# Kernel optimization log

Measured on AMD Instinct MI355X. Metric: run time of the kernel, lower is better.

Reference implementation:

```python
import jax, jax.numpy as jnp
import numpy as np

HEADS = 4


def _forward(x_atoms, pos, edge_attr, molecular_features, emb_W, emb_b, mp_W1, mp_b1, mp_W2, mp_b2, ln_g, ln_b, attn_in_w, attn_in_b, attn_out_w, attn_out_b, pool_W, pool_b, mol_gate, lrn_gate, molemb_W1, molemb_b1, molemb_W2, molemb_b2, lrnemb_W1, lrnemb_b1, lrnemb_W2, lrnemb_b2, fus_W1, fus_b1, fus_W2, fus_b2, head_W1, head_b1, head_W2, head_b2, edge_index, batch_idx):
    N = x_atoms.shape[0]
    B = molecular_features.shape[0]
    A = N // B  # equal-size molecules; batch_idx = repeat(arange(B), A)
    H = emb_W.shape[1]
    L = mp_W1.shape[0]
    src, dst = edge_index[0], edge_index[1]  # PyG: x_j = x[src], x_i = x[dst]
    x = x_atoms @ emb_W + emb_b
    # distance features (constant across layers)
    diff = pos[dst] - pos[src]
    d = jnp.sqrt(jnp.sum(diff * diff, axis=1, keepdims=True) + 1e-12)
    dist_feat = jnp.concatenate([d, 1.0 / (1.0 + d), jnp.exp(-d)], axis=1)  # [E,3]
    ones_e = jnp.ones((src.shape[0], 1), x.dtype)
    cnt = jnp.maximum(jax.ops.segment_sum(ones_e, dst, num_segments=N), 1.0)
    for l in range(L):
        res = x
        msg = jnp.concatenate([x[dst], x[src], dist_feat], axis=1)  # [E, 2H+3]
        msg = jax.nn.relu(msg @ mp_W1[l] + mp_b1[l]) @ mp_W2[l] + mp_b2[l]
        x = jax.ops.segment_sum(msg, dst, num_segments=N) / cnt  # mean aggregation
        y = x + res
        mu = y.mean(-1, keepdims=True)
        var = jnp.var(y, axis=-1, keepdims=True)
        x = (y - mu) * jax.lax.rsqrt(var + 1e-5) * ln_g[l] + ln_b[l]
    xm = x.reshape(B, A, H)
    explicit = xm.mean(axis=1)  # scatter_mean over equal-size graphs
    # per-molecule multi-head self-attention (torch MHA, eval mode)
    hd = H // HEADS
    qkv = xm @ attn_in_w.T + attn_in_b
    q, k, v = jnp.split(qkv, 3, axis=-1)
    q = q.reshape(B, A, HEADS, hd)
    k = k.reshape(B, A, HEADS, hd)
    v = v.reshape(B, A, HEADS, hd)
    scores = jnp.einsum('bqhd,bkhd->bhqk', q, k) / jnp.sqrt(jnp.asarray(hd, x.dtype))
    att = jax.nn.softmax(scores, axis=-1)
    o = jnp.einsum('bhqk,bkhd->bqhd', att, v).reshape(B, A, H)
    attended = o @ attn_out_w.T + attn_out_b
    aw = jax.nn.softmax(jnp.sum(attended * xm, axis=-1), axis=1)  # [B,A]
    wmean = jnp.sum(attended * aw[..., None], axis=1)
    maxp = attended.max(axis=1)
    meanp = attended.mean(axis=1)
    stdp = jnp.std(attended, axis=1, ddof=1)  # torch.std unbiased
    pooled = jnp.stack([wmean, maxp, meanp, stdp], axis=0)  # [4,B,H]
    proj = jnp.einsum('kbh,khf->kbf', pooled, pool_W) + pool_b[:, None, :]
    learned = jnp.moveaxis(proj, 0, 1).reshape(B, -1)  # [B,LF]
    # per-property gated MLPs, vectorized over P (atom gates are computed but unused in the source)
    gm = molecular_features[None] * jax.nn.sigmoid(mol_gate)[:, None, :]
    gl = learned[None] * jax.nn.sigmoid(lrn_gate)[:, None, :]
    molrep = jax.nn.relu(jnp.einsum('pbm,pmh->pbh', gm, molemb_W1) + molemb_b1[:, None, :])
    molrep = jnp.einsum('pbh,phk->pbk', molrep, molemb_W2) + molemb_b2[:, None, :]
    lrnrep = jax.nn.relu(jnp.einsum('pbm,pmh->pbh', gl, lrnemb_W1) + lrnemb_b1[:, None, :])
    lrnrep = jnp.einsum('pbh,phk->pbk', lrnrep, lrnemb_W2) + lrnemb_b2[:, None, :]
    P = mol_gate.shape[0]
    comb = jnp.concatenate([jnp.broadcast_to(explicit[None], (P, B, H)), molrep, lrnrep], axis=-1)
    fused = jax.nn.relu(jnp.einsum('pbc,pch->pbh', comb, fus_W1) + fus_b1[:, None, :])
    fused = jnp.einsum('pbh,phk->pbk', fused, fus_W2) + fus_b2[:, None, :]
    h = jax.nn.relu(jnp.einsum('pbh,phk->pbk', fused, head_W1) + head_b1[:, None, :])
    out = jnp.einsum('pbk,pko->pbo', h, head_W2) + head_b2[:, None, :]
    return out  # [P,B,1]: stacked predictions for the 4 properties


def setup_inputs() -> dict:
    key = jax.random.key(0)
    ks = jax.random.split(key, 24)
    B, A, F, M, H, LF, L, P = 1024, 32, 64, 200, 128, 64, 3, 4
    N = B * A
    E = N * 16
    H2, H4, Q = H // 2, H // 4, LF // 4
    n = lambda i, shape, s=1.0: jax.random.normal(ks[i], shape, dtype=jnp.float32) * s
    inp = {}
    inp['x_atoms'] = n(0, (N, F))
    inp['pos'] = n(1, (N, 3)) * 3.0
    inp['edge_attr'] = n(2, (E, 4))
    inp['molecular_features'] = n(3, (B, M))
    inp['emb_W'] = n(4, (F, H), 0.1)
    inp['emb_b'] = jnp.zeros((H,), jnp.float32)
    inp['mp_W1'] = n(5, (L, 2 * H + 3, H), 0.05)
    inp['mp_b1'] = jnp.zeros((L, H), jnp.float32)
    inp['mp_W2'] = n(6, (L, H, H), 0.05)
    inp['mp_b2'] = jnp.zeros((L, H), jnp.float32)
    inp['ln_g'] = jnp.ones((L, H), jnp.float32)
    inp['ln_b'] = jnp.zeros((L, H), jnp.float32)
    inp['attn_in_w'] = n(7, (3 * H, H), 0.08)
    inp['attn_in_b'] = jnp.zeros((3 * H,), jnp.float32)
    inp['attn_out_w'] = n(8, (H, H), 0.08)
    inp['attn_out_b'] = jnp.zeros((H,), jnp.float32)
    inp['pool_W'] = n(9, (4, H, Q), 0.08)
    inp['pool_b'] = jnp.zeros((4, Q), jnp.float32)
    inp['mol_gate'] = n(10, (P, M))
    inp['lrn_gate'] = n(11, (P, LF))
    inp['molemb_W1'] = n(12, (P, M, H2), 0.08)
    inp['molemb_b1'] = jnp.zeros((P, H2), jnp.float32)
    inp['molemb_W2'] = n(13, (P, H2, H2), 0.08)
    inp['molemb_b2'] = jnp.zeros((P, H2), jnp.float32)
    inp['lrnemb_W1'] = n(14, (P, LF, H2), 0.08)
    inp['lrnemb_b1'] = jnp.zeros((P, H2), jnp.float32)
    inp['lrnemb_W2'] = n(15, (P, H2, H2), 0.08)
    inp['lrnemb_b2'] = jnp.zeros((P, H2), jnp.float32)
    inp['fus_W1'] = n(16, (P, 2 * H, H), 0.08)
    inp['fus_b1'] = jnp.zeros((P, H), jnp.float32)
    inp['fus_W2'] = n(17, (P, H, H2), 0.08)
    inp['fus_b2'] = jnp.zeros((P, H2), jnp.float32)
    inp['head_W1'] = n(18, (P, H2, H4), 0.08)
    inp['head_b1'] = jnp.zeros((P, H4), jnp.float32)
    inp['head_W2'] = n(19, (P, H4, 1), 0.08)
    inp['head_b2'] = jnp.zeros((P, 1), jnp.float32)
    inp['edge_index'] = jax.random.randint(ks[20], (2, E), 0, N)
    inp['batch_idx'] = jnp.repeat(jnp.arange(B), A)
    return inp


def reference(x_atoms, pos, edge_attr, molecular_features, emb_W, emb_b, mp_W1, mp_b1, mp_W2, mp_b2, ln_g, ln_b, attn_in_w, attn_in_b, attn_out_w, attn_out_b, pool_W, pool_b, mol_gate, lrn_gate, molemb_W1, molemb_b1, molemb_W2, molemb_b2, lrnemb_W1, lrnemb_b1, lrnemb_W2, lrnemb_b2, fus_W1, fus_b1, fus_W2, fus_b2, head_W1, head_b1, head_W2, head_b2, edge_index, batch_idx):
    return _forward(x_atoms, pos, edge_attr, molecular_features, emb_W, emb_b, mp_W1, mp_b1, mp_W2, mp_b2, ln_g, ln_b, attn_in_w, attn_in_b, attn_out_w, attn_out_b, pool_W, pool_b, mol_gate, lrn_gate, molemb_W1, molemb_b1, molemb_W2, molemb_b2, lrnemb_W1, lrnemb_b1, lrnemb_W2, lrnemb_b2, fus_W1, fus_b1, fus_W2, fus_b2, head_W1, head_b1, head_W2, head_b2, edge_index, batch_idx)
```

## Files before the change

kernel.cpp:

```cpp
#include <hip/hip_runtime.h>

#define NE 524288
#define NN 32768
#define NB 1024

#define F4(p) (*(const float4*)(p))

typedef __bf16 bf16x8 __attribute__((ext_vector_type(8)));
typedef float  f32x4  __attribute__((ext_vector_type(4)));

__device__ __forceinline__ float sigmoidf_(float v) { return 1.f / (1.f + expf(-v)); }

__device__ __forceinline__ void bf16split(float f, short &hi, short &lo) {
  unsigned u = __float_as_uint(f);
  unsigned rh = (u + 0x7FFFu + ((u >> 16) & 1u)) >> 16;
  float fh = __uint_as_float(rh << 16);
  float fl = f - fh;
  unsigned u2 = __float_as_uint(fl);
  unsigned rl = (u2 + 0x7FFFu + ((u2 >> 16) & 1u)) >> 16;
  hi = (short)rh; lo = (short)rl;
}

__device__ __forceinline__ unsigned short f2bf(float f) {
  unsigned u = __float_as_uint(f);
  return (unsigned short)((u + 0x7FFFu + ((u >> 16) & 1u)) >> 16);
}
__device__ __forceinline__ float bf2f(unsigned short h) {
  return __uint_as_float(((unsigned)h) << 16);
}

__device__ __forceinline__ void ld32(float* xr, const float* p) {
#pragma unroll
  for (int i = 0; i < 32; i += 4) {
    float4 v = F4(&p[i]);
    xr[i] = v.x; xr[i+1] = v.y; xr[i+2] = v.z; xr[i+3] = v.w;
  }
}

__device__ __forceinline__ float dot32r(const float* __restrict__ w, const float* xr) {
  float s = 0.f;
#pragma unroll
  for (int i = 0; i < 32; i += 4) {
    float4 ww = F4(&w[i]);
    s = fmaf(xr[i],   ww.x, s);
    s = fmaf(xr[i+1], ww.y, s);
    s = fmaf(xr[i+2], ww.z, s);
    s = fmaf(xr[i+3], ww.w, s);
  }
  return s;
}

__global__ __launch_bounds__(256) void hist_kernel(const int* __restrict__ ei, int* __restrict__ cnt) {
  const int e = blockIdx.x*256 + threadIdx.x;
  atomicAdd(&cnt[ei[NE + e]], 1);
}

__global__ __launch_bounds__(1024) void scan_kernel(
    const int* __restrict__ cnt, int* __restrict__ off, int* __restrict__ cur)
{
  __shared__ int wsum[16];
  const int t = threadIdx.x;
  int local[32];
  const int base = t*32;
  int s = 0;
#pragma unroll
  for (int i = 0; i < 32; ++i) { local[i] = cnt[base+i]; s += local[i]; }
  int pre = s;
  const int lane = t & 63;
#pragma unroll
  for (int o = 1; o < 64; o <<= 1) { int v = __shfl_up(pre, o); if (lane >= o) pre += v; }
  if (lane == 63) wsum[t >> 6] = pre;
  __syncthreads();
  if (t == 0) { int a = 0; for (int w = 0; w < 16; ++w) { int v = wsum[w]; wsum[w] = a; a += v; } }
  __syncthreads();
  int excl = wsum[t >> 6] + pre - s;
#pragma unroll
  for (int i = 0; i < 32; ++i) { off[base+i] = excl; cur[base+i] = excl; excl += local[i]; }
  if (t == 1023) off[NN] = excl;
}

__global__ __launch_bounds__(256) void scatter_kernel(
    const float* __restrict__ pos, const int* __restrict__ ei,
    int* __restrict__ cur, float4* __restrict__ csr_rec)
{
  const int e = blockIdx.x*256 + threadIdx.x;
  const int s = ei[e];
  const int d = ei[NE + e];
  float dx = pos[d*3+0] - pos[s*3+0];
  float dy = pos[d*3+1] - pos[s*3+1];
  float dz = pos[d*3+2] - pos[s*3+2];
  float dist = sqrtf(dx*dx + dy*dy + dz*dz + 1e-12f);
  const int slot = atomicAdd(&cur[d], 1);
  csr_rec[slot] = make_float4(__int_as_float(s), dist, 1.f/(1.f + dist), expf(-dist));
}

__device__ __forceinline__ void pack_decode(int r, int N, int &k, int &n) {
  const int j = r & 7, lane = (r >> 3) & 63, rest = r >> 9;
  const int NT = N >> 4;
  const int t = rest % NT, kc = rest / NT;
  k = kc*32 + (lane >> 4)*8 + j;
  n = t*16 + (lane & 15);
}

#define W1AB_OFF 0
#define W2_OFF   98304
#define WIN_OFF  147456
#define WOUT_OFF 196608
#define EMB_OFF  212992
#define PK_TOTAL 221184

__global__ __launch_bounds__(256) void prep_kernel(
    const float* __restrict__ mp_W1, const float* __restrict__ mp_W2,
    const float* __restrict__ win, const float* __restrict__ wout,
    const float* __restrict__ emb_W, const float* __restrict__ mp_b1,
    short* __restrict__ bh, short* __restrict__ bl, float* __restrict__ pqbias)
{
  const int i = blockIdx.x*256 + threadIdx.x;
  if (i < 768) { const int l = i >> 8, t = i & 255; pqbias[i] = t < 128 ? mp_b1[l*128 + t] : 0.f; }
  if (i >= PK_TOTAL) return;
  int k, n; float v;
  if (i < W2_OFF) {
    const int l = i / 32768, r = i % 32768;
    pack_decode(r, 256, k, n);
    const float* W = mp_W1 + (size_t)l*259*128;
    v = (n < 128) ? W[k*128 + n] : W[(128+k)*128 + (n-128)];
  } else if (i < WIN_OFF) {
    const int q = i - W2_OFF, l = q / 16384, r = q % 16384;
    pack_decode(r, 128, k, n);
    v = mp_W2[(size_t)l*16384 + k*128 + n];
  } else if (i < WOUT_OFF) {
    pack_decode(i - WIN_OFF, 384, k, n);
    v = win[n*128 + k];
  } else if (i < EMB_OFF) {
    pack_decode(i - WOUT_OFF, 128, k, n);
    v = wout[n*128 + k];
  } else {
    pack_decode(i - EMB_OFF, 128, k, n);
    v = emb_W[k*128 + n];
  }
  short h_, lo; bf16split(v, h_, lo);
  bh[i] = h_; bl[i] = lo;
}

__global__ __launch_bounds__(256) void gate_prep_kernel(
    const float* __restrict__ meW1, const float* __restrict__ mol_gate,
    const float* __restrict__ leW1, const float* __restrict__ lrn_gate,
    float* __restrict__ meW1g, float* __restrict__ leW1g)
{
  const int i = blockIdx.x*256 + threadIdx.x;
  if (i < 51200) {
    const int p = i / 12800, r = i % 12800, k = r >> 6;
    meW1g[i] = meW1[i] * sigmoidf_(mol_gate[p*200 + k]);
  } else if (i < 67584) {
    const int q = i - 51200;
    const int p = q / 4096, r = q % 4096, k = r >> 6;
    leW1g[q] = leW1[q] * sigmoidf_(lrn_gate[p*64 + k]);
  }
}

__global__ __launch_bounds__(256, 2) void mfma_gemm_kernel(
    const float* __restrict__ A, int lda, int K,
    const short* __restrict__ Bh, const short* __restrict__ Bl,
    const float* __restrict__ bias, float* __restrict__ C, int ncols, int ldc,
    int relu, unsigned short* __restrict__ qbf)
{
  const int lane = threadIdx.x & 63, wid = threadIdx.x >> 6;
  const int m0 = blockIdx.x * 128 + wid * 32;
  const int n0 = blockIdx.y * 64;
  const int NT = ncols >> 4;
  const int cl = lane & 15, kg = lane >> 4;
  const int KC = K >> 5;

  f32x4 acc[2][4];
#pragma unroll
  for (int s = 0; s < 2; ++s)
#pragma unroll
    for (int t = 0; t < 4; ++t) acc[s][t] = (f32x4){0.f,0.f,0.f,0.f};

  for (int kc = 0; kc < KC; ++kc) {
    bf16x8 Ah[2], Al[2];
#pragma unroll
    for (int s = 0; s < 2; ++s) {
      const float* ap = &A[(size_t)(m0 + s*16 + cl)*lda + kc*32 + kg*8];
      const float4 f0 = F4(ap), f1 = F4(ap + 4);
      const float fv[8] = {f0.x,f0.y,f0.z,f0.w,f1.x,f1.y,f1.z,f1.w};
      union { short s[8]; bf16x8 b; } uh, ul;
#pragma unroll
      for (int j = 0; j < 8; ++j) bf16split(fv[j], uh.s[j], ul.s[j]);
      Ah[s] = uh.b; Al[s] = ul.b;
    }
    bf16x8 Bfh[4], Bfl[4];
#pragma unroll
    for (int t = 0; t < 4; ++t) {
      const size_t off = (((size_t)(kc*NT + (n0 >> 4) + t))*64 + lane)*8;
      Bfh[t] = *(const bf16x8*)&Bh[off];
      Bfl[t] = *(const bf16x8*)&Bl[off];
    }
#pragma unroll
    for (int s = 0; s < 2; ++s)
#pragma unroll
      for (int t = 0; t < 4; ++t)
        acc[s][t] = __builtin_amdgcn_mfma_f32_16x16x32_bf16(Ah[s], Bfh[t], acc[s][t], 0, 0, 0);
#pragma unroll
    for (int s = 0; s < 2; ++s)
#pragma unroll
      for (int t = 0; t < 4; ++t)
        acc[s][t] = __builtin_amdgcn_mfma_f32_16x16x32_bf16(Ah[s], Bfl[t], acc[s][t], 0, 0, 0);
#pragma unroll
    for (int s = 0; s < 2; ++s)
#pragma unroll
      for (int t = 0; t < 4; ++t)
        acc[s][t] = __builtin_amdgcn_mfma_f32_16x16x32_bf16(Al[s], Bfh[t], acc[s][t], 0, 0, 0);
  }

#pragma unroll
  for (int t = 0; t < 4; ++t) {
    const int col = n0 + t*16 + cl;
    const float bv = bias[col];
#pragma unroll
    for (int s = 0; s < 2; ++s) {
      const int rbase = m0 + s*16 + kg*4;
#pragma unroll
      for (int r = 0; r < 4; ++r) {
        float v = acc[s][t][r] + bv;
        if (relu) v = fmaxf(v, 0.f);
        if (qbf && col >= 128)
          qbf[(size_t)(rbase + r)*128 + (col - 128)] = f2bf(v);
        else
          C[(size_t)(rbase + r)*ldc + col] = v;
      }
    }
  }
}

__global__ __launch_bounds__(256, 2) void mfma_gemm_ln_kernel(
    const float* __restrict__ A, int lda,
    const short* __restrict__ Bh, const short* __restrict__ Bl,
    const float* __restrict__ b2, const int* __restrict__ csr_off,
    const float* __restrict__ g, const float* __restrict__ bb,
    float* __restrict__ x)
{
  const int lane = threadIdx.x & 63, wid = threadIdx.x >> 6;
  const int m0 = blockIdx.x * 64 + wid * 16;
  const int cl = lane & 15, kg = lane >> 4;

  bf16x8 Ah[4], Al[4];
#pragma unroll
  for (int kc = 0; kc < 4; ++kc) {
    const float* ap = &A[(size_t)(m0 + cl)*lda + kc*32 + kg*8];
    const float4 f0 = F4(ap), f1 = F4(ap + 4);
    const float fv[8] = {f0.x,f0.y,f0.z,f0.w,f1.x,f1.y,f1.z,f1.w};
    union { short s[8]; bf16x8 b; } uh, ul;
#pragma unroll
    for (int j = 0; j < 8; ++j) bf16split(fv[j], uh.s[j], ul.s[j]);
    Ah[kc] = uh.b; Al[kc] = ul.b;
  }

  f32x4 acc[8];
#pragma unroll
  for (int t = 0; t < 8; ++t) acc[t] = (f32x4){0.f,0.f,0.f,0.f};

#pragma unroll
  for (int kc = 0; kc < 4; ++kc) {
    bf16x8 Bfh[8], Bfl[8];
#pragma unroll
    for (int t = 0; t < 8; ++t) {
      const size_t off = (((size_t)(kc*8 + t))*64 + lane)*8;
      Bfh[t] = *(const bf16x8*)&Bh[off];
      Bfl[t] = *(const bf16x8*)&Bl[off];
    }
#pragma unroll
    for (int t = 0; t < 8; ++t)
      acc[t] = __builtin_amdgcn_mfma_f32_16x16x32_bf16(Ah[kc], Bfh[t], acc[t], 0, 0, 0);
#pragma unroll
    for (int t = 0; t < 8; ++t)
      acc[t] = __builtin_amdgcn_mfma_f32_16x16x32_bf16(Ah[kc], Bfl[t], acc[t], 0, 0, 0);
#pragma unroll
    for (int t = 0; t < 8; ++t)
      acc[t] = __builtin_amdgcn_mfma_f32_16x16x32_bf16(Al[kc], Bfh[t], acc[t], 0, 0, 0);
  }

  const int r0 = m0 + kg*4;
  float sflag[4];
#pragma unroll
  for (int r = 0; r < 4; ++r)
    sflag[r] = (csr_off[r0 + r + 1] > csr_off[r0 + r]) ? 1.f : 0.f;

  float ps[4] = {0.f,0.f,0.f,0.f}, pq[4] = {0.f,0.f,0.f,0.f};
  float yv[8][4];
#pragma unroll
  for (int t = 0; t < 8; ++t) {
    const int col = t*16 + cl;
    const float b2v = b2[col];
#pragma unroll
    for (int r = 0; r < 4; ++r) {
      const float y = acc[t][r] + sflag[r]*b2v + x[(size_t)(r0 + r)*128 + col];
      yv[t][r] = y;
      ps[r] += y;
      pq[r] = fmaf(y, y, pq[r]);
    }
  }
#pragma unroll
  for (int o = 1; o < 16; o <<= 1) {
#pragma unroll
    for (int r = 0; r < 4; ++r) { ps[r] += __shfl_xor(ps[r], o); pq[r] += __shfl_xor(pq[r], o); }
  }
#pragma unroll
  for (int r = 0; r < 4; ++r) {
    const float mu = ps[r] * (1.f/128.f);
    const float var = pq[r]*(1.f/128.f) - mu*mu;
    const float rstd = rsqrtf(var + 1e-5f);
#pragma unroll
    for (int t = 0; t < 8; ++t) {
      const int col = t*16 + cl;
      x[(size_t)(r0 + r)*128 + col] = (yv[t][r] - mu)*rstd*g[col] + bb[col];
    }
  }
}

__global__ __launch_bounds__(256, 6) void agg_kernel(
    float* __restrict__ P, const unsigned short* __restrict__ Qbf,
    const int* __restrict__ csr_off, const float4* __restrict__ csr_rec,
    const float* __restrict__ W1)
{
  const int tid = threadIdx.x;
  const int node = blockIdx.x*4 + (tid >> 6);
  const int lane = tid & 63;
  const int c0 = lane*2;
  const int off0 = csr_off[node], off1 = csr_off[node+1];

  const float* __restrict__ w1c = W1 + 256*128;
  const float w00 = w1c[c0],       w01 = w1c[c0+1];
  const float w10 = w1c[128+c0],   w11 = w1c[128+c0+1];
  const float w20 = w1c[256+c0],   w21 = w1c[256+c0+1];
  const float2 p = *(const float2*)&P[(size_t)node*128 + c0];

  float a0 = 0.f, a1 = 0.f;
  int e = off0;
  for (; e + 8 <= off1; e += 8) {
    float4 rc[8];
#pragma unroll
    for (int j = 0; j < 8; ++j) rc[j] = csr_rec[e+j];
    ushort2 qv[8];
#pragma unroll
    for (int j = 0; j < 8; ++j)
      qv[j] = *(const ushort2*)&Qbf[(size_t)__float_as_int(rc[j].x)*128 + c0];
#pragma unroll
    for (int j = 0; j < 8; ++j) {
      float h0 = p.x + bf2f(qv[j].x);
      h0 = fmaf(rc[j].y, w00, h0); h0 = fmaf(rc[j].z, w10, h0); h0 = fmaf(rc[j].w, w20, h0);
      float h1 = p.y + bf2f(qv[j].y);
      h1 = fmaf(rc[j].y, w01, h1); h1 = fmaf(rc[j].z, w11, h1); h1 = fmaf(rc[j].w, w21, h1);
      a0 += fmaxf(h0, 0.f);
      a1 += fmaxf(h1, 0.f);
    }
  }
  for (; e < off1; ++e) {
    const float4 rc = csr_rec[e];
    const ushort2 qv = *(const ushort2*)&Qbf[(size_t)__float_as_int(rc.x)*128 + c0];
    float h0 = p.x + bf2f(qv.x);
    h0 = fmaf(rc.y, w00, h0); h0 = fmaf(rc.z, w10, h0); h0 = fmaf(rc.w, w20, h0);
    float h1 = p.y + bf2f(qv.y);
    h1 = fmaf(rc.y, w01, h1); h1 = fmaf(rc.z, w11, h1); h1 = fmaf(rc.w, w21, h1);
    a0 += fmaxf(h0, 0.f);
    a1 += fmaxf(h1, 0.f);
  }
  const int deg = off1 - off0;
  const float rc_ = deg > 0 ? 1.f/(float)deg : 1.f;
  *(float2*)&P[(size_t)node*128 + c0] = make_float2(a0*rc_, a1*rc_);
}

__global__ __launch_bounds__(128) void attn_kernel(float* __restrict__ dqkv)
{
  __shared__ float sk[32*132];
  __shared__ float sv[32*132];
  const int tid = threadIdx.x;
  const int b = blockIdx.x;

  for (int idx = tid; idx < 1024; idx += 128) {
    const int a = idx >> 5, c4 = idx & 31;
    *(float4*)&sk[a*132 + c4*4] = F4(&dqkv[(size_t)(b*32+a)*384 + 128 + c4*4]);
    *(float4*)&sv[a*132 + c4*4] = F4(&dqkv[(size_t)(b*32+a)*384 + 256 + c4*4]);
  }
  __syncthreads();

  const int h = tid >> 5, qr = tid & 31;
  float qreg[32];
  ld32(qreg, &dqkv[(size_t)(b*32+qr)*384 + h*32]);

  float sc[32];
#pragma unroll
  for (int k = 0; k < 32; ++k)
    sc[k] = dot32r(&sk[k*132 + h*32], qreg) * 0.17677669529663687f;
  float mx = sc[0];
#pragma unroll
  for (int k = 1; k < 32; ++k) mx = fmaxf(mx, sc[k]);
  float se = 0.f;
#pragma unroll
  for (int k = 0; k < 32; ++k) { sc[k] = expf(sc[k] - mx); se += sc[k]; }
  const float inv = 1.f / se;

  __syncthreads();

  float od[32];
#pragma unroll
  for (int i = 0; i < 32; ++i) od[i] = 0.f;
#pragma unroll 4
  for (int k = 0; k < 32; ++k) {
    const float w = sc[k] * inv;
    const float* vr = &sv[k*132 + h*32];
#pragma unroll
    for (int i = 0; i < 32; i += 4) {
      float4 v = F4(&vr[i]);
      od[i]   = fmaf(w, v.x, od[i]);
      od[i+1] = fmaf(w, v.y, od[i+1]);
      od[i+2] = fmaf(w, v.z, od[i+2]);
      od[i+3] = fmaf(w, v.w, od[i+3]);
    }
  }
#pragma unroll
  for (int i = 0; i < 32; i += 4)
    *(float4*)&sk[qr*132 + h*32 + i] = make_float4(od[i], od[i+1], od[i+2], od[i+3]);
  __syncthreads();

  for (int idx = tid; idx < 1024; idx += 128) {
    const int a = idx >> 5, c4 = idx & 31;
    *(float4*)&dqkv[(size_t)(b*32+a)*384 + 256 + c4*4] = F4(&sk[a*132 + c4*4]);
  }
}

__global__ __launch_bounds__(256) void pool_head2_kernel(
    const float* __restrict__ att, const float* __restrict__ x,
    const float* __restrict__ pW, const float* __restrict__ pb,
    const float* __restrict__ molf,
    const float* __restrict__ meW1g, const float* __restrict__ meb1,
    const float* __restrict__ meW2, const float* __restrict__ meb2,
    const float* __restrict__ leW1g, const float* __restrict__ leb1,
    const float* __restrict__ leW2, const float* __restrict__ leb2,
    const float* __restrict__ fW1, const float* __restrict__ fb1,
    const float* __restrict__ fW2, const float* __restrict__ fb2,
    const float* __restrict__ hW1, const float* __restrict__ hb1,
    const float* __restrict__ hW2, const float* __restrict__ hb2,
    float* __restrict__ out)
{
  const int b2 = blockIdx.x * 2, tid = threadIdx.x;
  __shared__ float satt[8448];
  __shared__ float sx[8448];
  __shared__ float aw_l[64];
  __shared__ float spool[1024];
  __shared__ float slrn[128];
  __shared__ float sexpl[256];
  __shared__ float smolf[400];

  for (int idx = tid; idx < 2048; idx += 256) {
    const int m = idx >> 10, r = idx & 1023;
    const int a = r >> 5, c4 = r & 31;
    *(float4*)&satt[m*4224 + a*132 + c4*4] = F4(&att[(size_t)((b2+m)*32+a)*128 + c4*4]);
    *(float4*)&sx[m*4224 + a*132 + c4*4]   = F4(&x[(size_t)((b2+m)*32+a)*128 + c4*4]);
  }
  for (int i = tid; i < 400; i += 256) {
    const int m = i / 200, k = i - m*200;
    smolf[i] = molf[(size_t)(b2+m)*200 + k];
  }
  __syncthreads();

  const int hh = tid >> 7, t2 = tid & 127;

  {
    const int a = t2 >> 2, q4 = t2 & 3;
    const float* sa = &satt[hh*4224 + a*132 + q4*32];
    const float* sb = &sx[hh*4224 + a*132 + q4*32];
    float sp = 0.f;
#pragma unroll
    for (int i = 0; i < 32; ++i) sp = fmaf(sa[i], sb[i], sp);
    sp += __shfl_xor(sp, 1);
    sp += __shfl_xor(sp, 2);
    if (q4 == 0) aw_l[hh*32 + a] = sp;
  }
  __syncthreads();

  {
    float awr[32];
    float mxl = aw_l[hh*32];
#pragma unroll
    for (int a = 1; a < 32; ++a) mxl = fmaxf(mxl, aw_l[hh*32 + a]);
    float se = 0.f;
#pragma unroll
    for (int a = 0; a < 32; ++a) { awr[a] = expf(aw_l[hh*32 + a] - mxl); se += awr[a]; }
    const float inv = 1.f / se;
    const int c = t2;
    float mx = -3.4e38f, sm = 0.f, wm = 0.f, ex = 0.f;
#pragma unroll
    for (int a = 0; a < 32; ++a) {
      const float v = satt[hh*4224 + a*132 + c];
      mx = fmaxf(mx, v);
      sm += v;
      wm = fmaf(v, awr[a], wm);
      ex += sx[hh*4224 + a*132 + c];
    }
    wm *= inv;
    const float mean = sm * 0.03125f;
    float s2 = 0.f;
#pragma unroll
    for (int a = 0; a < 32; ++a) {
      const float d = satt[hh*4224 + a*132 + c] - mean;
      s2 = fmaf(d, d, s2);
    }
    const float stdp = sqrtf(s2 * (1.f/31.f));
    sexpl[hh*128 + c]       = ex * 0.03125f;
    spool[hh*512 + c]       = wm;
    spool[hh*512 + 128 + c] = mx;
    spool[hh*512 + 256 + c] = mean;
    spool[hh*512 + 384 + c] = stdp;
  }
  __syncthreads();

  if (t2 < 64) {
    const int k = t2 >> 4, qq = t2 & 15;
    const float* pk = pW + k*2048;
    const float* sp_ = &spool[hh*512 + k*128];
    float s0 = 0.f, s1 = 0.f, s2 = 0.f, s3 = 0.f;
    for (int h2 = 0; h2 < 128; h2 += 4) {
      s0 = fmaf(sp_[h2],   pk[h2*16 + qq],     s0);
      s1 = fmaf(sp_[h2+1], pk[(h2+1)*16 + qq], s1);
      s2 = fmaf(sp_[h2+2], pk[(h2+2)*16 + qq], s2);
      s3 = fmaf(sp_[h2+3], pk[(h2+3)*16 + qq], s3);
    }
    slrn[hh*64 + t2] = pb[k*16 + qq] + (s0+s1) + (s2+s3);
  }
  __syncthreads();

  const int p = tid >> 6, l = tid & 63;

  float m1_0, m1_1;
  {
    const float* w = meW1g + p*12800 + l;
    float a0[8] = {0,0,0,0,0,0,0,0}, a1[8] = {0,0,0,0,0,0,0,0};
    for (int k = 0; k < 200; k += 8) {
      float wv[8], u0[8], u1[8];
#pragma unroll
      for (int j = 0; j < 8; ++j) wv[j] = w[(k+j)*64];
#pragma unroll
      for (int j = 0; j < 8; ++j) { u0[j] = smolf[k+j]; u1[j] = smolf[200+k+j]; }
#pragma unroll
      for (int j = 0; j < 8; ++j) {
        a0[j] = fmaf(u0[j], wv[j], a0[j]);
        a1[j] = fmaf(u1[j], wv[j], a1[j]);
      }
    }
    const float bv = meb1[p*64 + l];
    m1_0 = fmaxf(((a0[0]+a0[1])+(a0[2]+a0[3])) + ((a0[4]+a0[5])+(a0[6]+a0[7])) + bv, 0.f);
    m1_1 = fmaxf(((a1[0]+a1[1])+(a1[2]+a1[3])) + ((a1[4]+a1[5])+(a1[6]+a1[7])) + bv, 0.f);
  }
  float l1_0, l1_1;
  {
    const float* w = leW1g + p*4096 + l;
    float a0[8] = {0,0,0,0,0,0,0,0}, a1[8] = {0,0,0,0,0,0,0,0};
    for (int k = 0; k < 64; k += 8) {
      float wv[8], u0[8], u1[8];
#pragma unroll
      for (int j = 0; j < 8; ++j) wv[j] = w[(k+j)*64];
#pragma unroll
      for (int j = 0; j < 8; ++j) { u0[j] = slrn[k+j]; u1[j] = slrn[64+k+j]; }
#pragma unroll
      for (int j = 0; j < 8; ++j) {
        a0[j] = fmaf(u0[j], wv[j], a0[j]);
        a1[j] = fmaf(u1[j], wv[j], a1[j]);
      }
    }
    const float bv = leb1[p*64 + l];
    l1_0 = fmaxf(((a0[0]+a0[1])+(a0[2]+a0[3])) + ((a0[4]+a0[5])+(a0[6]+a0[7])) + bv, 0.f);
    l1_1 = fmaxf(((a1[0]+a1[1])+(a1[2]+a1[3])) + ((a1[4]+a1[5])+(a1[6]+a1[7])) + bv, 0.f);
  }
  float m2_0, m2_1;
  {
    const float* w = meW2 + p*4096 + l;
    float a0[8] = {0,0,0,0,0,0,0,0}, a1[8] = {0,0,0,0,0,0,0,0};
    for (int k = 0; k < 64; k += 8) {
      float wv[8], u0[8], u1[8];
#pragma unroll
      for (int j = 0; j < 8; ++j) wv[j] = w[(k+j)*64];
#pragma unroll
      for (int j = 0; j < 8; ++j) { u0[j] = __shfl(m1_0, k+j); u1[j] = __shfl(m1_1, k+j); }
#pragma unroll
      for (int j = 0; j < 8; ++j) {
        a0[j] = fmaf(u0[j], wv[j], a0[j]);
        a1[j] = fmaf(u1[j], wv[j], a1[j]);
      }
    }
    const float bv = meb2[p*64 + l];
    m2_0 = ((a0[0]+a0[1])+(a0[2]+a0[3])) + ((a0[4]+a0[5])+(a0[6]+a0[7])) + bv;
    m2_1 = ((a1[0]+a1[1])+(a1[2]+a1[3])) + ((a1[4]+a1[5])+(a1[6]+a1[7])) + bv;
  }
  float l2_0, l2_1;
  {
    const float* w = leW2 + p*4096 + l;
    float a0[8] = {0,0,0,0,0,0,0,0}, a1[8] = {0,0,0,0,0,0,0,0};
    for (int k = 0; k < 64; k += 8) {
      float wv[8], u0[8], u1[8];
#pragma unroll
      for (int j = 0; j < 8; ++j) wv[j] = w[(k+j)*64];
#pragma unroll
      for (int j = 0; j < 8; ++j) { u0[j] = __shfl(l1_0, k+j); u1[j] = __shfl(l1_1, k+j); }
#pragma unroll
      for (int j = 0; j < 8; ++j) {
        a0[j] = fmaf(u0[j], wv[j], a0[j]);
        a1[j] = fmaf(u1[j], wv[j], a1[j]);
      }
    }
    const float bv = leb2[p*64 + l];
    l2_0 = ((a0[0]+a0[1])+(a0[2]+a0[3])) + ((a0[4]+a0[5])+(a0[6]+a0[7])) + bv;
    l2_1 = ((a1[0]+a1[1])+(a1[2]+a1[3])) + ((a1[4]+a1[5])+(a1[6]+a1[7])) + bv;
  }
  float f1a_0, f1a_1, f1b_0, f1b_1;
  {
    const float* w = fW1 + p*32768;
    float a0[8]={0,0,0,0,0,0,0,0}, a1[8]={0,0,0,0,0,0,0,0};
    float c0[8]={0,0,0,0,0,0,0,0}, c1[8]={0,0,0,0,0,0,0,0};
    for (int k = 0; k < 128; k += 8) {
      float w0[8], w1[8], u0[8], u1[8];
#pragma unroll
      for (int j = 0; j < 8; ++j) w0[j] = w[(k+j)*128 + l];
#pragma unroll
      for (int j = 0; j < 8; ++j) w1[j] = w[(k+j)*128 + 64 + l];
#pragma unroll
      for (int j = 0; j < 8; ++j) { u0[j] = sexpl[k+j]; u1[j] = sexpl[128+k+j]; }
#pragma unroll
      for (int j = 0; j < 8; ++j) {
        a0[j] = fmaf(u0[j], w0[j], a0[j]);  a1[j] = fmaf(u1[j], w0[j], a1[j]);
        c0[j] = fmaf(u0[j], w1[j], c0[j]);  c1[j] = fmaf(u1[j], w1[j], c1[j]);
      }
    }
    for (int k = 0; k < 64; k += 8) {
      float w0[8], w1[8], u0[8], u1[8];
#pragma unroll
      for (int j = 0; j < 8; ++j) w0[j] = w[(128+k+j)*128 + l];
#pragma unroll
      for (int j = 0; j < 8; ++j) w1[j] = w[(128+k+j)*128 + 64 + l];
#pragma unroll
      for (int j = 0; j < 8; ++j) { u0[j] = __shfl(m2_0, k+j); u1[j] = __shfl(m2_1, k+j); }
#pragma unroll
      for (int j = 0; j < 8; ++j) {
        a0[j] = fmaf(u0[j], w0[j], a0[j]);  a1[j] = fmaf(u1[j], w0[j], a1[j]);
        c0[j] = fmaf(u0[j], w1[j], c0[j]);  c1[j] = fmaf(u1[j], w1[j], c1[j]);
      }
    }
    for (int k = 0; k < 64; k += 8) {
      float w0[8], w1[8], u0[8], u1[8];
#pragma unroll
      for (int j = 0; j < 8; ++j) w0[j] = w[(192+k+j)*128 + l];
#pragma unroll
      for (int j = 0; j < 8; ++j) w1[j] = w[(192+k+j)*128 + 64 + l];
#pragma unroll
      for (int j = 0; j < 8; ++j) { u0[j] = __shfl(l2_0, k+j); u1[j] = __shfl(l2_1, k+j); }
#pragma unroll
      for (int j = 0; j < 8; ++j) {
        a0[j] = fmaf(u0[j], w0[j], a0[j]);  a1[j] = fmaf(u1[j], w0[j], a1[j]);
        c0[j] = fmaf(u0[j], w1[j], c0[j]);  c1[j] = fmaf(u1[j], w1[j], c1[j]);
      }
    }
    const float ba = fb1[p*128 + l], bc = fb1[p*128 + 64 + l];
    f1a_0 = fmaxf(((a0[0]+a0[1])+(a0[2]+a0[3])) + ((a0[4]+a0[5])+(a0[6]+a0[7])) + ba, 0.f);
    f1a_1 = fmaxf(((a1[0]+a1[1])+(a1[2]+a1[3])) + ((a1[4]+a1[5])+(a1[6]+a1[7])) + ba, 0.f);
    f1b_0 = fmaxf(((c0[0]+c0[1])+(c0[2]+c0[3])) + ((c0[4]+c0[5])+(c0[6]+c0[7])) + bc, 0.f);
    f1b_1 = fmaxf(((c1[0]+c1[1])+(c1[2]+c1[3])) + ((c1[4]+c1[5])+(c1[6]+c1[7])) + bc, 0.f);
  }
  float f2_0, f2_1;
  {
    const float* w = fW2 + p*8192 + l;
    float a0[8]={0,0,0,0,0,0,0,0}, a1[8]={0,0,0,0,0,0,0,0};
    for (int k = 0; k < 64; k += 8) {
      float wv[8], u0[8], u1[8];
#pragma unroll
      for (int j = 0; j < 8; ++j) wv[j] = w[(k+j)*64];
#pragma unroll
      for (int j = 0; j < 8; ++j) { u0[j] = __shfl(f1a_0, k+j); u1[j] = __shfl(f1a_1, k+j); }
#pragma unroll
      for (int j = 0; j < 8; ++j) {
        a0[j] = fmaf(u0[j], wv[j], a0[j]);
        a1[j] = fmaf(u1[j], wv[j], a1[j]);
      }
    }
    for (int k = 0; k < 64; k += 8) {
      float wv[8], u0[8], u1[8];
#pragma unroll
      for (int j = 0; j < 8; ++j) wv[j] = w[(64+k+j)*64];
#pragma unroll
      for (int j = 0; j < 8; ++j) { u0[j] = __shfl(f1b_0, k+j); u1[j] = __shfl(f1b_1, k+j); }
#pragma unroll
      for (int j = 0; j < 8; ++j) {
        a0[j] = fmaf(u0[j], wv[j], a0[j]);
        a1[j] = fmaf(u1[j], wv[j], a1[j]);
      }
    }
    const float bv = fb2[p*64 + l];
    f2_0 = ((a0[0]+a0[1])+(a0[2]+a0[3])) + ((a0[4]+a0[5])+(a0[6]+a0[7])) + bv;
    f2_1 = ((a1[0]+a1[1])+(a1[2]+a1[3])) + ((a1[4]+a1[5])+(a1[6]+a1[7])) + bv;
  }
  {
    const float* w = hW1 + p*2048 + (l & 31);
    float a0[8]={0,0,0,0,0,0,0,0}, a1[8]={0,0,0,0,0,0,0,0};
    for (int k = 0; k < 64; k += 8) {
      float wv[8], u0[8], u1[8];
#pragma unroll
      for (int j = 0; j < 8; ++j) wv[j] = w[(k+j)*32];
#pragma unroll
      for (int j = 0; j < 8; ++j) { u0[j] = __shfl(f2_0, k+j); u1[j] = __shfl(f2_1, k+j); }
#pragma unroll
      for (int j = 0; j < 8; ++j) {
        a0[j] = fmaf(u0[j], wv[j], a0[j]);
        a1[j] = fmaf(u1[j], wv[j], a1[j]);
      }
    }
    float v0 = 0.f, v1 = 0.f;
    if (l < 32) {
      const float hb = hb1[p*32 + l], w2v = hW2[p*32 + l];
      v0 = fmaxf(((a0[0]+a0[1])+(a0[2]+a0[3])) + ((a0[4]+a0[5])+(a0[6]+a0[7])) + hb, 0.f) * w2v;
      v1 = fmaxf(((a1[0]+a1[1])+(a1[2]+a1[3])) + ((a1[4]+a1[5])+(a1[6]+a1[7])) + hb, 0.f) * w2v;
    }
#pragma unroll
    for (int o = 1; o < 32; o <<= 1) { v0 += __shfl_xor(v0, o); v1 += __shfl_xor(v1, o); }
    if (l == 0) {
      const float hb2v = hb2[p];
      out[p*1024 + b2 + 0] = v0 + hb2v;
      out[p*1024 + b2 + 1] = v1 + hb2v;
    }
  }
}

extern "C" void kernel_launch(void* const* d_in, const int* in_sizes, int n_in,
                              void* d_out, int out_size, void* d_ws, size_t ws_size,
                              hipStream_t stream) {
  const float* x_atoms    = (const float*)d_in[0];
  const float* pos        = (const float*)d_in[1];
  const float* molf       = (const float*)d_in[3];
  const float* emb_W      = (const float*)d_in[4];
  const float* emb_b      = (const float*)d_in[5];
  const float* mp_W1      = (const float*)d_in[6];
  const float* mp_b1      = (const float*)d_in[7];
  const float* mp_W2      = (const float*)d_in[8];
  const float* mp_b2      = (const float*)d_in[9];
  const float* ln_g       = (const float*)d_in[10];
  const float* ln_b       = (const float*)d_in[11];
  const float* attn_in_w  = (const float*)d_in[12];
  const float* attn_in_b  = (const float*)d_in[13];
  const float* attn_out_w = (const float*)d_in[14];
  const float* attn_out_b = (const float*)d_in[15];
  const float* pool_W     = (const float*)d_in[16];
  const float* pool_b     = (const float*)d_in[17];
  const float* mol_gate   = (const float*)d_in[18];
  const float* lrn_gate   = (const float*)d_in[19];
  const float* meW1       = (const float*)d_in[20];
  const float* meb1       = (const float*)d_in[21];
  const float* meW2       = (const float*)d_in[22];
  const float* meb2       = (const float*)d_in[23];
  const float* leW1       = (const float*)d_in[24];
  const float* leb1       = (const float*)d_in[25];
  const float* leW2       = (const float*)d_in[26];
  const float* leb2       = (const float*)d_in[27];
  const float* fW1        = (const float*)d_in[28];
  const float* fb1        = (const float*)d_in[29];
  const float* fW2        = (const float*)d_in[30];
  const float* fb2        = (const float*)d_in[31];
  const float* hW1        = (const float*)d_in[32];
  const float* hb1        = (const float*)d_in[33];
  const float* hW2        = (const float*)d_in[34];
  const float* hb2        = (const float*)d_in[35];
  const int*   ei         = (const int*)d_in[36];

  float* ws      = (float*)d_ws;
  float* x       = ws;
  float* region  = x + (size_t)NN*128;
  float* P       = region;
  unsigned short* Qbf = (unsigned short*)(region + (size_t)NN*128);
  float* dqkv    = region;
  float* att     = region + (size_t)NN*384;
  float* csr_rf  = att + (size_t)NN*128;
  float4* csr_rec = (float4*)csr_rf;
  int*   cnt_i   = (int*)(csr_rf + (size_t)NE*4);
  int*   csr_off = cnt_i + NN;
  int*   cur     = csr_off + NN + 64;
  float* pqbias  = (float*)(cur + NN);
  short* bh      = (short*)(pqbias + 768);
  short* bl      = bh + PK_TOTAL;
  float* meW1g   = (float*)(bl + PK_TOTAL);
  float* leW1g   = meW1g + 51200;

  hipMemsetAsync(cnt_i, 0, (size_t)NN*sizeof(int), stream);

  prep_kernel<<<(PK_TOTAL + 255)/256, 256, 0, stream>>>(
      mp_W1, mp_W2, attn_in_w, attn_out_w, emb_W, mp_b1, bh, bl, pqbias);
  gate_prep_kernel<<<(67584 + 255)/256, 256, 0, stream>>>(
      meW1, mol_gate, leW1, lrn_gate, meW1g, leW1g);
  hist_kernel<<<NE/256, 256, 0, stream>>>(ei, cnt_i);
  scan_kernel<<<1, 1024, 0, stream>>>(cnt_i, csr_off, cur);
  scatter_kernel<<<NE/256, 256, 0, stream>>>(pos, ei, cur, csr_rec);

  mfma_gemm_kernel<<<dim3(NN/128, 2), 256, 0, stream>>>(
      x_atoms, 64, 64, bh + EMB_OFF, bl + EMB_OFF, emb_b, x, 128, 128, 0, nullptr);

  for (int l = 0; l < 3; ++l) {
    mfma_gemm_kernel<<<dim3(NN/128, 4), 256, 0, stream>>>(
        x, 128, 128, bh + W1AB_OFF + l*32768, bl + W1AB_OFF + l*32768,
        pqbias + l*256, P, 256, 128, 0, Qbf);
    agg_kernel<<<NN/4, 256, 0, stream>>>(P, Qbf, csr_off, csr_rec,
                                         mp_W1 + (size_t)l*259*128);
    mfma_gemm_ln_kernel<<<NN/64, 256, 0, stream>>>(
        P, 128, bh + W2_OFF + l*16384, bl + W2_OFF + l*16384,
        mp_b2 + l*128, csr_off, ln_g + l*128, ln_b + l*128, x);
  }

  mfma_gemm_kernel<<<dim3(NN/128, 6), 256, 0, stream>>>(
      x, 128, 128, bh + WIN_OFF, bl + WIN_OFF, attn_in_b, dqkv, 384, 384, 0, nullptr);
  attn_kernel<<<NB, 128, 0, stream>>>(dqkv);
  mfma_gemm_kernel<<<dim3(NN/128, 2), 256, 0, stream>>>(
      dqkv + 256, 384, 128, bh + WOUT_OFF, bl + WOUT_OFF, attn_out_b, att, 128, 128, 0, nullptr);

  pool_head2_kernel<<<NB/2, 256, 0, stream>>>(
      att, x, pool_W, pool_b, molf,
      meW1g, meb1, meW2, meb2, leW1g, leb1, leW2, leb2,
      fW1, fb1, fW2, fb2, hW1, hb1, hW2, hb2, (float*)d_out);
}
```

Measured before the change: 383.9 us.

## Store activations pre-split into bf16 hi/lo planes for downstream GEMMs

Producers of x and the aggregated messages (embedding GEMM, LayerNorm GEMM, aggregation kernel) now also write bf16 hi/lo split copies. Consumer GEMMs read these planes directly instead of loading fp32 and splitting per tile. This removes the repeated split arithmetic in the GEMM inner loops, which was duplicated across the N-dimension blocks, and keeps the total bytes read the same. In exchange, producers issue extra scalar 16-bit stores and the workspace grows. The relu option is removed from the generic GEMM.

```diff
diff --git a/kernel.cpp b/kernel.cpp
--- a/kernel.cpp
+++ b/kernel.cpp
@@ -162,7 +162,7 @@
     const float* __restrict__ A, int lda, int K,
     const short* __restrict__ Bh, const short* __restrict__ Bl,
     const float* __restrict__ bias, float* __restrict__ C, int ncols, int ldc,
-    int relu, unsigned short* __restrict__ qbf)
+    unsigned short* __restrict__ sh, unsigned short* __restrict__ sl)
 {
   const int lane = threadIdx.x & 63, wid = threadIdx.x >> 6;
   const int m0 = blockIdx.x * 128 + wid * 32;
@@ -222,8 +222,80 @@
       const int rbase = m0 + s*16 + kg*4;
 #pragma unroll
       for (int r = 0; r < 4; ++r) {
-        float v = acc[s][t][r] + bv;
-        if (relu) v = fmaxf(v, 0.f);
+        const float v = acc[s][t][r] + bv;
+        C[(size_t)(rbase + r)*ldc + col] = v;
+        if (sh) {
+          short hh_, ll_;
+          bf16split(v, hh_, ll_);
+          sh[(size_t)(rbase + r)*128 + col] = (unsigned short)hh_;
+          sl[(size_t)(rbase + r)*128 + col] = (unsigned short)ll_;
+        }
+      }
+    }
+  }
+}
+
+__global__ __launch_bounds__(256, 2) void mfma_gemm_s_kernel(
+    const unsigned short* __restrict__ Ah_, const unsigned short* __restrict__ Al_,
+    const short* __restrict__ Bh, const short* __restrict__ Bl,
+    const float* __restrict__ bias, float* __restrict__ C, int ncols, int ldc,
+    unsigned short* __restrict__ qbf)
+{
+  const int lane = threadIdx.x & 63, wid = threadIdx.x >> 6;
+  const int m0 = blockIdx.x * 128 + wid * 32;
+  const int n0 = blockIdx.y * 64;
+  const int NT = ncols >> 4;
+  const int cl = lane & 15, kg = lane >> 4;
+
+  f32x4 acc[2][4];
+#pragma unroll
+  for (int s = 0; s < 2; ++s)
+#pragma unroll
+    for (int t = 0; t < 4; ++t) acc[s][t] = (f32x4){0.f,0.f,0.f,0.f};
+
+#pragma unroll
+  for (int kc = 0; kc < 4; ++kc) {
+    bf16x8 Ah[2], Al[2];
+#pragma unroll
+    for (int s = 0; s < 2; ++s) {
+      const size_t ro = (size_t)(m0 + s*16 + cl)*128 + kc*32 + kg*8;
+      Ah[s] = *(const bf16x8*)&Ah_[ro];
+      Al[s] = *(const bf16x8*)&Al_[ro];
+    }
+    bf16x8 Bfh[4], Bfl[4];
+#pragma unroll
+    for (int t = 0; t < 4; ++t) {
+      const size_t off = (((size_t)(kc*NT + (n0 >> 4) + t))*64 + lane)*8;
+      Bfh[t] = *(const bf16x8*)&Bh[off];
+      Bfl[t] = *(const bf16x8*)&Bl[off];
+    }
+#pragma unroll
+    for (int s = 0; s < 2; ++s)
+#pragma unroll
+      for (int t = 0; t < 4; ++t)
+        acc[s][t] = __builtin_amdgcn_mfma_f32_16x16x32_bf16(Ah[s], Bfh[t], acc[s][t], 0, 0, 0);
+#pragma unroll
+    for (int s = 0; s < 2; ++s)
+#pragma unroll
+      for (int t = 0; t < 4; ++t)
+        acc[s][t] = __builtin_amdgcn_mfma_f32_16x16x32_bf16(Ah[s], Bfl[t], acc[s][t], 0, 0, 0);
+#pragma unroll
+    for (int s = 0; s < 2; ++s)
+#pragma unroll
+      for (int t = 0; t < 4; ++t)
+        acc[s][t] = __builtin_amdgcn_mfma_f32_16x16x32_bf16(Al[s], Bfh[t], acc[s][t], 0, 0, 0);
+  }
+
+#pragma unroll
+  for (int t = 0; t < 4; ++t) {
+    const int col = n0 + t*16 + cl;
+    const float bv = bias[col];
+#pragma unroll
+    for (int s = 0; s < 2; ++s) {
+      const int rbase = m0 + s*16 + kg*4;
+#pragma unroll
+      for (int r = 0; r < 4; ++r) {
+        const float v = acc[s][t][r] + bv;
         if (qbf && col >= 128)
           qbf[(size_t)(rbase + r)*128 + (col - 128)] = f2bf(v);
         else
@@ -233,12 +305,12 @@
   }
 }
 
-__global__ __launch_bounds__(256, 2) void mfma_gemm_ln_kernel(
-    const float* __restrict__ A, int lda,
+__global__ __launch_bounds__(256, 2) void mfma_gemm_ln_s_kernel(
+    const unsigned short* __restrict__ Ah_, const unsigned short* __restrict__ Al_,
     const short* __restrict__ Bh, const short* __restrict__ Bl,
     const float* __restrict__ b2, const int* __restrict__ csr_off,
     const float* __restrict__ g, const float* __restrict__ bb,
-    float* __restrict__ x)
+    float* __restrict__ x, unsigned short* __restrict__ xh, unsigned short* __restrict__ xl)
 {
   const int lane = threadIdx.x & 63, wid = threadIdx.x >> 6;
   const int m0 = blockIdx.x * 64 + wid * 16;
@@ -247,13 +319,9 @@
   bf16x8 Ah[4], Al[4];
 #pragma unroll
   for (int kc = 0; kc < 4; ++kc) {
-    const float* ap = &A[(size_t)(m0 + cl)*lda + kc*32 + kg*8];
-    const float4 f0 = F4(ap), f1 = F4(ap + 4);
-    const float fv[8] = {f0.x,f0.y,f0.z,f0.w,f1.x,f1.y,f1.z,f1.w};
-    union { short s[8]; bf16x8 b; } uh, ul;
-#pragma unroll
-    for (int j = 0; j < 8; ++j) bf16split(fv[j], uh.s[j], ul.s[j]);
-    Ah[kc] = uh.b; Al[kc] = ul.b;
+    const size_t ro = (size_t)(m0 + cl)*128 + kc*32 + kg*8;
+    Ah[kc] = *(const bf16x8*)&Ah_[ro];
+    Al[kc] = *(const bf16x8*)&Al_[ro];
   }
 
   f32x4 acc[8];
@@ -313,15 +381,22 @@
 #pragma unroll
     for (int t = 0; t < 8; ++t) {
       const int col = t*16 + cl;
-      x[(size_t)(r0 + r)*128 + col] = (yv[t][r] - mu)*rstd*g[col] + bb[col];
+      const float o_ = (yv[t][r] - mu)*rstd*g[col] + bb[col];
+      const size_t idx = (size_t)(r0 + r)*128 + col;
+      x[idx] = o_;
+      short hh_, ll_;
+      bf16split(o_, hh_, ll_);
+      xh[idx] = (unsigned short)hh_;
+      xl[idx] = (unsigned short)ll_;
     }
   }
 }
 
 __global__ __launch_bounds__(256, 6) void agg_kernel(
-    float* __restrict__ P, const unsigned short* __restrict__ Qbf,
+    const float* __restrict__ P, const unsigned short* __restrict__ Qbf,
     const int* __restrict__ csr_off, const float4* __restrict__ csr_rec,
-    const float* __restrict__ W1)
+    const float* __restrict__ W1,
+    unsigned short* __restrict__ Ph, unsigned short* __restrict__ Pl)
 {
   const int tid = threadIdx.x;
   const int node = blockIdx.x*4 + (tid >> 6);
@@ -367,7 +442,11 @@
   }
   const int deg = off1 - off0;
   const float rc_ = deg > 0 ? 1.f/(float)deg : 1.f;
-  *(float2*)&P[(size_t)node*128 + c0] = make_float2(a0*rc_, a1*rc_);
+  short h0_, l0_, h1_, l1_;
+  bf16split(a0*rc_, h0_, l0_);
+  bf16split(a1*rc_, h1_, l1_);
+  *(ushort2*)&Ph[(size_t)node*128 + c0] = make_ushort2((unsigned short)h0_, (unsigned short)h1_);
+  *(ushort2*)&Pl[(size_t)node*128 + c0] = make_ushort2((unsigned short)l0_, (unsigned short)l1_);
 }
 
 __global__ __launch_bounds__(128) void attn_kernel(float* __restrict__ dqkv)
@@ -773,6 +852,8 @@
   float* region  = x + (size_t)NN*128;
   float* P       = region;
   unsigned short* Qbf = (unsigned short*)(region + (size_t)NN*128);
+  unsigned short* Ph  = (unsigned short*)(region + (size_t)NN*192);
+  unsigned short* Pl  = (unsigned short*)(region + (size_t)NN*256);
   float* dqkv    = region;
   float* att     = region + (size_t)NN*384;
   float* csr_rf  = att + (size_t)NN*128;
@@ -785,6 +866,8 @@
   short* bl      = bh + PK_TOTAL;
   float* meW1g   = (float*)(bl + PK_TOTAL);
   float* leW1g   = meW1g + 51200;
+  unsigned short* xh = (unsigned short*)(leW1g + 16384);
+  unsigned short* xl = xh + (size_t)NN*128;
 
   hipMemsetAsync(cnt_i, 0, (size_t)NN*sizeof(int), stream);
 
@@ -797,24 +880,25 @@
   scatter_kernel<<<NE/256, 256, 0, stream>>>(pos, ei, cur, csr_rec);
 
   mfma_gemm_kernel<<<dim3(NN/128, 2), 256, 0, stream>>>(
-      x_atoms, 64, 64, bh + EMB_OFF, bl + EMB_OFF, emb_b, x, 128, 128, 0, nullptr);
+      x_atoms, 64, 64, bh + EMB_OFF, bl + EMB_OFF, emb_b, x, 128, 128, xh, xl);
 
   for (int l = 0; l < 3; ++l) {
-    mfma_gemm_kernel<<<dim3(NN/128, 4), 256, 0, stream>>>(
-        x, 128, 128, bh + W1AB_OFF + l*32768, bl + W1AB_OFF + l*32768,
-        pqbias + l*256, P, 256, 128, 0, Qbf);
+    mfma_gemm_s_kernel<<<dim3(NN/128, 4), 256, 0, stream>>>(
+        xh, xl, bh + W1AB_OFF + l*32768, bl + W1AB_OFF + l*32768,
+        pqbias + l*256, P, 256, 128, Qbf);
     agg_kernel<<<NN/4, 256, 0, stream>>>(P, Qbf, csr_off, csr_rec,
-                                         mp_W1 + (size_t)l*259*128);
-    mfma_gemm_ln_kernel<<<NN/64, 256, 0, stream>>>(
-        P, 128, bh + W2_OFF + l*16384, bl + W2_OFF + l*16384,
-        mp_b2 + l*128, csr_off, ln_g + l*128, ln_b + l*128, x);
-  }
-
-  mfma_gemm_kernel<<<dim3(NN/128, 6), 256, 0, stream>>>(
-      x, 128, 128, bh + WIN_OFF, bl + WIN_OFF, attn_in_b, dqkv, 384, 384, 0, nullptr);
+                                         mp_W1 + (size_t)l*259*128, Ph, Pl);
+    mfma_gemm_ln_s_kernel<<<NN/64, 256, 0, stream>>>(
+        Ph, Pl, bh + W2_OFF + l*16384, bl + W2_OFF + l*16384,
+        mp_b2 + l*128, csr_off, ln_g + l*128, ln_b + l*128, x, xh, xl);
+  }
+
+  mfma_gemm_s_kernel<<<dim3(NN/128, 6), 256, 0, stream>>>(
+      xh, xl, bh + WIN_OFF, bl + WIN_OFF, attn_in_b, dqkv, 384, 384, nullptr);
   attn_kernel<<<NB, 128, 0, stream>>>(dqkv);
   mfma_gemm_kernel<<<dim3(NN/128, 2), 256, 0, stream>>>(
-      dqkv + 256, 384, 128, bh + WOUT_OFF, bl + WOUT_OFF, attn_out_b, att, 128, 128, 0, nullptr);
+      dqkv + 256, 384, 128, bh + WOUT_OFF, bl + WOUT_OFF, attn_out_b, att, 128, 128,
+      nullptr, nullptr);
 
   pool_head2_kernel<<<NB/2, 256, 0, stream>>>(
       att, x, pool_W, pool_b, molf,
```

Result: slower. 398.8 us (+3.9%).
